# Performance work log

Measured on AMD Instinct MI355X. Metric: run time of the kernel, lower is better.

The kernel has to match this reference:

```python
import jax, jax.numpy as jnp
import numpy as np

RES = 64
FDIM = 32
BOUNDS = (-1.0, 1.0)


def _bilinear_sample(plane, gx, gy):
    """plane: [C,H,W]; gx,gy: [N] grid coords in [-1,1].
    Matches F.grid_sample(align_corners=True, mode='bilinear', padding_mode='border').
    gx indexes width (last dim), gy indexes height. Returns [N, C]."""
    C, H, W = plane.shape
    x = (gx + 1.0) * 0.5 * (W - 1)  # pixel coords
    y = (gy + 1.0) * 0.5 * (H - 1)
    x0 = jnp.floor(x)
    y0 = jnp.floor(y)
    wx = x - x0
    wy = y - y0
    x0i = jnp.clip(x0, 0, W - 1).astype(jnp.int32)
    x1i = jnp.clip(x0 + 1, 0, W - 1).astype(jnp.int32)
    y0i = jnp.clip(y0, 0, H - 1).astype(jnp.int32)
    y1i = jnp.clip(y0 + 1, 0, H - 1).astype(jnp.int32)
    # gathers: [C, N]
    v00 = plane[:, y0i, x0i]
    v01 = plane[:, y0i, x1i]
    v10 = plane[:, y1i, x0i]
    v11 = plane[:, y1i, x1i]
    top = v00 * (1.0 - wx) + v01 * wx
    bot = v10 * (1.0 - wx) + v11 * wx
    return (top * (1.0 - wy) + bot * wy).T  # [N, C]


def setup_inputs() -> dict:
    key = jax.random.key(0)
    k_xyz, k_xy, k_xz, k_yz = jax.random.split(key, 4)
    N = 2_000_000
    xyz = jax.random.normal(k_xyz, (N, 3), dtype=jnp.float32)
    # xavier_uniform on [1, C, R, R]: fan_in = fan_out = C*R*R -> bound = sqrt(6/(2*C*R*R))
    bound = float(np.sqrt(6.0 / (2.0 * FDIM * RES * RES)))
    def plane(k):
        return jax.random.uniform(k, (FDIM, RES, RES), dtype=jnp.float32,
                                  minval=-bound, maxval=bound)
    return {
        "xyz": xyz,
        "plane_xy": plane(k_xy),
        "plane_xz": plane(k_xz),
        "plane_yz": plane(k_yz),
    }


def reference(xyz, plane_xy, plane_xz, plane_yz):
    lo, hi = BOUNDS
    g = 2.0 * (xyz - lo) / (hi - lo) - 1.0
    g = jnp.clip(g, -1.0, 1.0)
    x, y, z = g[:, 0], g[:, 1], g[:, 2]
    feat_xy = _bilinear_sample(plane_xy, x, y)
    feat_xz = _bilinear_sample(plane_xz, x, z)
    feat_yz = _bilinear_sample(plane_yz, y, z)
    return jnp.concatenate([feat_xy, feat_xz, feat_yz], axis=-1)  # [N, 3*FDIM]
```

## Files before the change

kernel.cpp:

```cpp
#include <hip/hip_runtime.h>
#include <hip/hip_bf16.h>

#define RES 64
#define FDIM 32
#define PLANE_ELEMS (FDIM * RES * RES)

typedef float vfloat4 __attribute__((ext_vector_type(4)));

__global__ void transpose_planes_bf16(const float* __restrict__ p0,
                                      const float* __restrict__ p1,
                                      const float* __restrict__ p2,
                                      __hip_bfloat16* __restrict__ out) {
    int i = blockIdx.x * blockDim.x + threadIdx.x;
    if (i >= 3 * PLANE_ELEMS) return;
    int p  = i / PLANE_ELEMS;
    int r  = i - p * PLANE_ELEMS;
    int c  = r & (FDIM - 1);
    int yx = r >> 5;
    const float* in = (p == 0) ? p0 : (p == 1) ? p1 : p2;
    out[i] = __float2bfloat16(in[c * (RES * RES) + yx]);
}

__device__ __forceinline__ void grid_coord(float g, int& i0, int& i1, float& w) {
    g = fminf(fmaxf(g, -1.0f), 1.0f);
    float u = (g + 1.0f) * 0.5f * (float)(RES - 1);
    float f = floorf(u);
    w = u - f;
    int ii = (int)f;
    ii = ii < 0 ? 0 : (ii > RES - 1 ? RES - 1 : ii);
    i0 = ii;
    i1 = ii + 1 > RES - 1 ? RES - 1 : ii + 1;
}

__device__ __forceinline__ vfloat4 dec4(uint2 w) {
    vfloat4 f;
    f.x = __uint_as_float(w.x << 16);
    f.y = __uint_as_float(w.x & 0xffff0000u);
    f.z = __uint_as_float(w.y << 16);
    f.w = __uint_as_float(w.y & 0xffff0000u);
    return f;
}

__device__ __forceinline__ vfloat4 bilerp4(uint2 w00, uint2 w01, uint2 w10,
                                           uint2 w11, float wx, float wy) {
    vfloat4 v00 = dec4(w00), v01 = dec4(w01), v10 = dec4(w10), v11 = dec4(w11);
    float iwx = 1.0f - wx, iwy = 1.0f - wy;
    vfloat4 top = v00 * iwx + v01 * wx;
    vfloat4 bot = v10 * iwx + v11 * wx;
    return top * iwy + bot * wy;
}

__global__ __launch_bounds__(256) void kplanes_sample_bf16(
    const float* __restrict__ xyz,
    const __hip_bfloat16* __restrict__ planes_t,
    float* __restrict__ out, int N) {
    int tid = blockIdx.x * blockDim.x + threadIdx.x;
    int pt = tid >> 3;
    int cg = tid & 7;
    if (pt >= N) return;

    float gx = xyz[pt * 3 + 0];
    float gy = xyz[pt * 3 + 1];
    float gz = xyz[pt * 3 + 2];

    int x0, x1, y0, y1, z0, z1;
    float wx, wy, wz;
    grid_coord(gx, x0, x1, wx);
    grid_coord(gy, y0, y1, wy);
    grid_coord(gz, z0, z1, wz);

    const uint2* P = (const uint2*)planes_t;
    vfloat4* o = (vfloat4*)out;
    long long orow = (long long)pt * 24 + cg;

    {
        uint2 w00 = P[(y0 * RES + x0) * 8 + cg];
        uint2 w01 = P[(y0 * RES + x1) * 8 + cg];
        uint2 w10 = P[(y1 * RES + x0) * 8 + cg];
        uint2 w11 = P[(y1 * RES + x1) * 8 + cg];
        vfloat4 r = bilerp4(w00, w01, w10, w11, wx, wy);
        __builtin_nontemporal_store(r, &o[orow]);
    }
    {
        const uint2* B = P + 4096 * 8;
        uint2 w00 = B[(z0 * RES + x0) * 8 + cg];
        uint2 w01 = B[(z0 * RES + x1) * 8 + cg];
        uint2 w10 = B[(z1 * RES + x0) * 8 + cg];
        uint2 w11 = B[(z1 * RES + x1) * 8 + cg];
        vfloat4 r = bilerp4(w00, w01, w10, w11, wx, wz);
        __builtin_nontemporal_store(r, &o[orow + 8]);
    }
    {
        const uint2* B = P + 2 * 4096 * 8;
        uint2 w00 = B[(z0 * RES + y0) * 8 + cg];
        uint2 w01 = B[(z0 * RES + y1) * 8 + cg];
        uint2 w10 = B[(z1 * RES + y0) * 8 + cg];
        uint2 w11 = B[(z1 * RES + y1) * 8 + cg];
        vfloat4 r = bilerp4(w00, w01, w10, w11, wy, wz);
        __builtin_nontemporal_store(r, &o[orow + 16]);
    }
}

__global__ __launch_bounds__(256) void kplanes_sample_chw(
    const float* __restrict__ xyz,
    const float* __restrict__ pxy,
    const float* __restrict__ pxz,
    const float* __restrict__ pyz,
    float* __restrict__ out, int N) {
    int tid = blockIdx.x * blockDim.x + threadIdx.x;
    int pt = tid >> 3;
    int cg = tid & 7;
    if (pt >= N) return;

    float gx = xyz[pt * 3 + 0];
    float gy = xyz[pt * 3 + 1];
    float gz = xyz[pt * 3 + 2];

    int x0, x1, y0, y1, z0, z1;
    float wx, wy, wz;
    grid_coord(gx, x0, x1, wx);
    grid_coord(gy, y0, y1, wy);
    grid_coord(gz, z0, z1, wz);

    long long obase = (long long)pt * 96 + cg * 4;

    const float* planes[3] = {pxy, pxz, pyz};
    int a0[3] = {y0 * RES + x0, z0 * RES + x0, z0 * RES + y0};
    int a1[3] = {y0 * RES + x1, z0 * RES + x1, z0 * RES + y1};
    int a2[3] = {y1 * RES + x0, z1 * RES + x0, z1 * RES + y0};
    int a3[3] = {y1 * RES + x1, z1 * RES + x1, z1 * RES + y1};
    float wwx[3] = {wx, wx, wy};
    float wwy[3] = {wy, wz, wz};

#pragma unroll
    for (int p = 0; p < 3; ++p) {
        const float* B = planes[p];
#pragma unroll
        for (int k = 0; k < 4; ++k) {
            int c = cg * 4 + k;
            const float* Bc = B + c * (RES * RES);
            float v00 = Bc[a0[p]];
            float v01 = Bc[a1[p]];
            float v10 = Bc[a2[p]];
            float v11 = Bc[a3[p]];
            float top = v00 * (1.0f - wwx[p]) + v01 * wwx[p];
            float bot = v10 * (1.0f - wwx[p]) + v11 * wwx[p];
            out[obase + p * 32 + k] = top * (1.0f - wwy[p]) + bot * wwy[p];
        }
    }
}

extern "C" void kernel_launch(void* const* d_in, const int* in_sizes, int n_in,
                              void* d_out, int out_size, void* d_ws, size_t ws_size,
                              hipStream_t stream) {
    const float* xyz = (const float*)d_in[0];
    const float* pxy = (const float*)d_in[1];
    const float* pxz = (const float*)d_in[2];
    const float* pyz = (const float*)d_in[3];
    float* out = (float*)d_out;
    int N = in_sizes[0] / 3;

    size_t need = (size_t)3 * PLANE_ELEMS * sizeof(__hip_bfloat16);
    long long total = (long long)N * 8;
    int grid = (int)((total + 255) / 256);

    if (ws_size >= need) {
        __hip_bfloat16* ws = (__hip_bfloat16*)d_ws;
        transpose_planes_bf16<<<(3 * PLANE_ELEMS + 255) / 256, 256, 0, stream>>>(
            pxy, pxz, pyz, ws);
        kplanes_sample_bf16<<<grid, 256, 0, stream>>>(xyz, ws, out, N);
    } else {
        kplanes_sample_chw<<<grid, 256, 0, stream>>>(xyz, pxy, pxz, pyz, out, N);
    }
}
```

Before: 145.8 us.

## Pack four bilinear corners per cell contiguously in bf16 texture

Builds a per-cell texture where each grid cell stores its four clamped corner feature vectors (bf16, 32 channels each) contiguously, so a sample reads one contiguous 256-byte block per plane instead of four scattered 64-byte rows. This cuts address computation and aims to reduce cache lines touched per point. In exchange the prep texture is four times larger (about 3 MB), which adds build cost and cache footprint.

```diff
diff --git a/kernel.cpp b/kernel.cpp
--- a/kernel.cpp
+++ b/kernel.cpp
@@ -3,33 +3,38 @@
 
 #define RES 64
 #define FDIM 32
-#define PLANE_ELEMS (FDIM * RES * RES)
+#define CELLS_PER_PLANE (RES * RES)
+#define CELL_ELEMS (4 * FDIM)
+#define TEX_ELEMS (3 * CELLS_PER_PLANE * CELL_ELEMS)
 
 typedef float vfloat4 __attribute__((ext_vector_type(4)));
 
-__global__ void transpose_planes_bf16(const float* __restrict__ p0,
-                                      const float* __restrict__ p1,
-                                      const float* __restrict__ p2,
-                                      __hip_bfloat16* __restrict__ out) {
-    int i = blockIdx.x * blockDim.x + threadIdx.x;
-    if (i >= 3 * PLANE_ELEMS) return;
-    int p  = i / PLANE_ELEMS;
-    int r  = i - p * PLANE_ELEMS;
-    int c  = r & (FDIM - 1);
-    int yx = r >> 5;
+__global__ void build_celltex(const float* __restrict__ p0,
+                              const float* __restrict__ p1,
+                              const float* __restrict__ p2,
+                              __hip_bfloat16* __restrict__ out) {
+    int e = blockIdx.x * blockDim.x + threadIdx.x;
+    if (e >= TEX_ELEMS) return;
+    int p      = e / (CELLS_PER_PLANE * CELL_ELEMS);
+    int r      = e - p * (CELLS_PER_PLANE * CELL_ELEMS);
+    int cell   = r >> 7;
+    int corner = (r >> 5) & 3;
+    int ch     = r & (FDIM - 1);
+    int y0 = cell >> 6;
+    int x0 = cell & 63;
+    int y = (corner & 2) ? (y0 + 1 > RES - 1 ? RES - 1 : y0 + 1) : y0;
+    int x = (corner & 1) ? (x0 + 1 > RES - 1 ? RES - 1 : x0 + 1) : x0;
     const float* in = (p == 0) ? p0 : (p == 1) ? p1 : p2;
-    out[i] = __float2bfloat16(in[c * (RES * RES) + yx]);
+    out[e] = __float2bfloat16(in[ch * (RES * RES) + y * RES + x]);
 }
 
-__device__ __forceinline__ void grid_coord(float g, int& i0, int& i1, float& w) {
+__device__ __forceinline__ void grid_coord(float g, int& i0, float& w) {
     g = fminf(fmaxf(g, -1.0f), 1.0f);
     float u = (g + 1.0f) * 0.5f * (float)(RES - 1);
     float f = floorf(u);
     w = u - f;
     int ii = (int)f;
-    ii = ii < 0 ? 0 : (ii > RES - 1 ? RES - 1 : ii);
-    i0 = ii;
-    i1 = ii + 1 > RES - 1 ? RES - 1 : ii + 1;
+    i0 = ii < 0 ? 0 : (ii > RES - 1 ? RES - 1 : ii);
 }
 
 __device__ __forceinline__ vfloat4 dec4(uint2 w) {
@@ -50,9 +55,9 @@
     return top * iwy + bot * wy;
 }
 
-__global__ __launch_bounds__(256) void kplanes_sample_bf16(
+__global__ __launch_bounds__(256) void kplanes_sample_celltex(
     const float* __restrict__ xyz,
-    const __hip_bfloat16* __restrict__ planes_t,
+    const __hip_bfloat16* __restrict__ tex,
     float* __restrict__ out, int N) {
     int tid = blockIdx.x * blockDim.x + threadIdx.x;
     int pt = tid >> 3;
@@ -63,42 +68,30 @@
     float gy = xyz[pt * 3 + 1];
     float gz = xyz[pt * 3 + 2];
 
-    int x0, x1, y0, y1, z0, z1;
+    int x0, y0, z0;
     float wx, wy, wz;
-    grid_coord(gx, x0, x1, wx);
-    grid_coord(gy, y0, y1, wy);
-    grid_coord(gz, z0, z1, wz);
+    grid_coord(gx, x0, wx);
+    grid_coord(gy, y0, wy);
+    grid_coord(gz, z0, wz);
 
-    const uint2* P = (const uint2*)planes_t;
+    const uint2* T = (const uint2*)tex;
+    const uint2* A = T + ((            (y0 << 6) + x0) << 5) + cg;
+    const uint2* B = T + ((CELLS_PER_PLANE     + (z0 << 6) + x0) << 5) + cg;
+    const uint2* C = T + ((2 * CELLS_PER_PLANE + (z0 << 6) + y0) << 5) + cg;
+
+    uint2 a00 = A[0], a01 = A[8], a10 = A[16], a11 = A[24];
+    uint2 b00 = B[0], b01 = B[8], b10 = B[16], b11 = B[24];
+    uint2 c00 = C[0], c01 = C[8], c10 = C[16], c11 = C[24];
+
     vfloat4* o = (vfloat4*)out;
     long long orow = (long long)pt * 24 + cg;
 
-    {
-        uint2 w00 = P[(y0 * RES + x0) * 8 + cg];
-        uint2 w01 = P[(y0 * RES + x1) * 8 + cg];
-        uint2 w10 = P[(y1 * RES + x0) * 8 + cg];
-        uint2 w11 = P[(y1 * RES + x1) * 8 + cg];
-        vfloat4 r = bilerp4(w00, w01, w10, w11, wx, wy);
-        __builtin_nontemporal_store(r, &o[orow]);
-    }
-    {
-        const uint2* B = P + 4096 * 8;
-        uint2 w00 = B[(z0 * RES + x0) * 8 + cg];
-        uint2 w01 = B[(z0 * RES + x1) * 8 + cg];
-        uint2 w10 = B[(z1 * RES + x0) * 8 + cg];
-        uint2 w11 = B[(z1 * RES + x1) * 8 + cg];
-        vfloat4 r = bilerp4(w00, w01, w10, w11, wx, wz);
-        __builtin_nontemporal_store(r, &o[orow + 8]);
-    }
-    {
-        const uint2* B = P + 2 * 4096 * 8;
-        uint2 w00 = B[(z0 * RES + y0) * 8 + cg];
-        uint2 w01 = B[(z0 * RES + y1) * 8 + cg];
-        uint2 w10 = B[(z1 * RES + y0) * 8 + cg];
-        uint2 w11 = B[(z1 * RES + y1) * 8 + cg];
-        vfloat4 r = bilerp4(w00, w01, w10, w11, wy, wz);
-        __builtin_nontemporal_store(r, &o[orow + 16]);
-    }
+    vfloat4 r0 = bilerp4(a00, a01, a10, a11, wx, wy);
+    __builtin_nontemporal_store(r0, &o[orow]);
+    vfloat4 r1 = bilerp4(b00, b01, b10, b11, wx, wz);
+    __builtin_nontemporal_store(r1, &o[orow + 8]);
+    vfloat4 r2 = bilerp4(c00, c01, c10, c11, wy, wz);
+    __builtin_nontemporal_store(r2, &o[orow + 16]);
 }
 
 __global__ __launch_bounds__(256) void kplanes_sample_chw(
@@ -116,11 +109,14 @@
     float gy = xyz[pt * 3 + 1];
     float gz = xyz[pt * 3 + 2];
 
-    int x0, x1, y0, y1, z0, z1;
+    int x0, y0, z0;
     float wx, wy, wz;
-    grid_coord(gx, x0, x1, wx);
-    grid_coord(gy, y0, y1, wy);
-    grid_coord(gz, z0, z1, wz);
+    grid_coord(gx, x0, wx);
+    grid_coord(gy, y0, wy);
+    grid_coord(gz, z0, wz);
+    int x1 = x0 + 1 > RES - 1 ? RES - 1 : x0 + 1;
+    int y1 = y0 + 1 > RES - 1 ? RES - 1 : y0 + 1;
+    int z1 = z0 + 1 > RES - 1 ? RES - 1 : z0 + 1;
 
     long long obase = (long long)pt * 96 + cg * 4;
 
@@ -134,11 +130,11 @@
 
 #pragma unroll
     for (int p = 0; p < 3; ++p) {
-        const float* B = planes[p];
+        const float* Bp = planes[p];
 #pragma unroll
         for (int k = 0; k < 4; ++k) {
             int c = cg * 4 + k;
-            const float* Bc = B + c * (RES * RES);
+            const float* Bc = Bp + c * (RES * RES);
             float v00 = Bc[a0[p]];
             float v01 = Bc[a1[p]];
             float v10 = Bc[a2[p]];
@@ -160,15 +156,15 @@
     float* out = (float*)d_out;
     int N = in_sizes[0] / 3;
 
-    size_t need = (size_t)3 * PLANE_ELEMS * sizeof(__hip_bfloat16);
+    size_t need = (size_t)TEX_ELEMS * sizeof(__hip_bfloat16);
     long long total = (long long)N * 8;
     int grid = (int)((total + 255) / 256);
 
     if (ws_size >= need) {
         __hip_bfloat16* ws = (__hip_bfloat16*)d_ws;
-        transpose_planes_bf16<<<(3 * PLANE_ELEMS + 255) / 256, 256, 0, stream>>>(
+        build_celltex<<<(TEX_ELEMS + 255) / 256, 256, 0, stream>>>(
             pxy, pxz, pyz, ws);
-        kplanes_sample_bf16<<<grid, 256, 0, stream>>>(xyz, ws, out, N);
+        kplanes_sample_celltex<<<grid, 256, 0, stream>>>(xyz, ws, out, N);
     } else {
         kplanes_sample_chw<<<grid, 256, 0, stream>>>(xyz, pxy, pxz, pyz, out, N);
     }
```

New measurement: 146.2 us. No clear change (+0.3%).
